# Optimization experiments

Hardware: AMD Instinct MI355X
Metric: run time of the kernel (lower is better)

## Reference

```python
import jax, jax.numpy as jnp
import numpy as np

B, C, H, W = 4, 512, 28, 28
HEADS, K, DIL = 16, 7, 1
DH = C // HEADS
EPS = 1e-5


def _nbr_idx(n):
    # NATTEN-style clamped windows: near borders the window shifts to stay in-bounds.
    span = DIL * (K - 1) + 1
    start = np.clip(np.arange(n) - (K // 2) * DIL, 0, n - span)
    idx = start[:, None] + np.arange(K) * DIL              # [n, K] absolute neighbor indices
    rel = (idx - np.arange(n)[:, None]) // DIL + (K - 1)    # [n, K] rpb indices in [0, 2K-2]
    return jnp.asarray(idx), jnp.asarray(rel)


def _batchnorm(x, gamma, beta):
    # x: [B, C, H, W]; training-mode BN (batch statistics, biased variance)
    mean = x.mean(axis=(0, 2, 3), keepdims=True)
    var = x.var(axis=(0, 2, 3), keepdims=True)
    xn = (x - mean) * jax.lax.rsqrt(var + EPS)
    return xn * gamma[None, :, None, None] + beta[None, :, None, None]


def _neighborhood_attn(xh, qkv_w, qkv_b, proj_w, proj_b, rpb):
    # xh: [B, H, W, C]
    qkv = jnp.einsum('bijc,oc->bijo', xh, qkv_w) + qkv_b          # [B,H,W,3C]
    qkv = qkv.reshape(B, H, W, 3, HEADS, DH)
    q = qkv[..., 0, :, :].transpose(0, 3, 1, 2, 4)                 # [B,heads,H,W,dh]
    k = qkv[..., 1, :, :].transpose(0, 3, 1, 2, 4)
    v = qkv[..., 2, :, :].transpose(0, 3, 1, 2, 4)

    idx_r, rel_r = _nbr_idx(H)
    idx_c, rel_c = _nbr_idx(W)

    def gather(t):  # [B,heads,H,W,dh] -> [B,heads,H,W,K*K,dh]
        t = t[:, :, idx_r]                 # [B,heads,H,K,W,dh]
        t = t[:, :, :, :, idx_c]           # [B,heads,H,K,W,K,dh]
        t = t.transpose(0, 1, 2, 4, 3, 5, 6)
        return t.reshape(B, HEADS, H, W, K * K, DH)

    kg = gather(k)
    vg = gather(v)

    scale = DH ** -0.5
    logits = jnp.einsum('bhijd,bhijnd->bhijn', q * scale, kg)      # [B,heads,H,W,K*K]

    # relative position bias: rpb[h, rel_r[i,a], rel_c[j,b]]
    bias = rpb[:, rel_r]                   # [heads,H,K,2K-1]
    bias = bias[:, :, :, rel_c]            # [heads,H,K,W,K]
    bias = bias.transpose(0, 1, 3, 2, 4).reshape(HEADS, H, W, K * K)
    logits = logits + bias[None]

    attn = jax.nn.softmax(logits, axis=-1)
    out = jnp.einsum('bhijn,bhijnd->bhijd', attn, vg)              # [B,heads,H,W,dh]
    out = out.transpose(0, 2, 3, 1, 4).reshape(B, H, W, C)
    return jnp.einsum('bijc,oc->bijo', out, proj_w) + proj_b


def setup_inputs() -> dict:
    key = jax.random.key(0)
    ks = jax.random.split(key, 8)
    p = lambda k_, shp: (jax.random.normal(k_, shp, jnp.float32) * 0.02)
    return {
        'x': jax.random.normal(ks[0], (B, C, H, W), jnp.float32),
        'qkv_w': p(ks[1], (3 * C, C)), 'qkv_b': jnp.zeros((3 * C,), jnp.float32),
        'proj_w': p(ks[2], (C, C)), 'proj_b': jnp.zeros((C,), jnp.float32),
        'rpb': p(ks[3], (HEADS, 2 * K - 1, 2 * K - 1)),
        'w1': p(ks[4], (2 * C, C)), 'b1': jnp.zeros((2 * C,), jnp.float32),
        'w2': p(ks[5], (C, 2 * C)), 'b2': jnp.zeros((C,), jnp.float32),
        'g1': jnp.ones((C,), jnp.float32), 'be1': jnp.zeros((C,), jnp.float32),
        'g2': jnp.ones((C,), jnp.float32), 'be2': jnp.zeros((C,), jnp.float32),
    }


def reference(x, qkv_w, qkv_b, proj_w, proj_b, rpb, w1, b1, w2, b2, g1, be1, g2, be2):
    xh = x.transpose(0, 2, 3, 1)                                   # NCHW -> NHWC
    h = _neighborhood_attn(xh, qkv_w, qkv_b, proj_w, proj_b, rpb)
    h = h.transpose(0, 3, 1, 2)                                    # back to NCHW
    x1 = _batchnorm(x + h, g1, be1)
    # FFN: 1x1 conv (C -> 2C), exact GELU, 1x1 conv (2C -> C)
    t = jnp.einsum('bchw,oc->bohw', x1, w1) + b1[None, :, None, None]
    t = jax.nn.gelu(t, approximate=False)
    h2 = jnp.einsum('bchw,oc->bohw', t, w2) + b2[None, :, None, None]
    return _batchnorm(x1 + h2, g2, be2)
```

## Files before the change

kernel.cpp:

```cpp
#include <hip/hip_runtime.h>
#include <hip/hip_bf16.h>
#include <math.h>

#define BATCH 4
#define CCH   512
#define HWPIX 784
#define NPIX  3136
#define MPAD  3200
#define EPS   1e-5f

using f32x4  = __attribute__((ext_vector_type(4))) float;
using bf16x8 = __attribute__((ext_vector_type(8))) __bf16;

__device__ __forceinline__ short f2b(float f) {
    unsigned u = __float_as_uint(f);
    unsigned r = (u + 0x7FFFu + ((u >> 16) & 1u)) >> 16;
    return (short)r;
}
__device__ __forceinline__ unsigned pk2(float a, float b) {
    return (unsigned)(unsigned short)f2b(a) | ((unsigned)(unsigned short)f2b(b) << 16);
}
__device__ __forceinline__ float bl(unsigned u)  { return __uint_as_float(u << 16); }
__device__ __forceinline__ float bh(unsigned u)  { return __uint_as_float(u & 0xffff0000u); }
__device__ __forceinline__ float b16f(short s) {
    return __uint_as_float((unsigned)(unsigned short)s << 16);
}

__device__ __forceinline__ void gload_lds16(const void* g, void* l) {
    __builtin_amdgcn_global_load_lds((const __attribute__((address_space(1))) void*)g,
                                     (__attribute__((address_space(3))) void*)l, 16, 0, 0);
}

__global__ __launch_bounds__(256) void k_prep(const float* __restrict__ qkv_w,
                                              const float* __restrict__ proj_w,
                                              const float* __restrict__ w2,
                                              const float* __restrict__ x,
                                              short* __restrict__ Wb,
                                              short* __restrict__ xhb) {
    __shared__ float tile[32][33];
    const int bid = blockIdx.x;
    if (bid < 1536) {
        int i = (bid * 256 + threadIdx.x) * 4;
        const float* src; int base;
        if (i < 786432)       { src = qkv_w;  base = 0; }
        else if (i < 1048576) { src = proj_w; base = 786432; }
        else                  { src = w2;     base = 1048576; }
        float4 v = *(const float4*)&src[i - base];
        *(uint2*)&Wb[i] = make_uint2(pk2(v.x, v.y), pk2(v.z, v.w));
        return;
    }
    const int t = bid - 1536;
    const int b = t / 400, r = t % 400;
    const int c0 = (r / 25) * 32, p0 = (r % 25) * 32;
    const int tx = threadIdx.x & 31, ty = threadIdx.x >> 5;
    for (int i = ty; i < 32; i += 8) {
        int c = c0 + i, p = p0 + tx;
        tile[i][tx] = (p < HWPIX) ? x[((size_t)b * CCH + c) * HWPIX + p] : 0.f;
    }
    __syncthreads();
    for (int i = ty; i < 32; i += 8) {
        int p = p0 + i, c = c0 + tx;
        if (p < HWPIX) xhb[((size_t)b * HWPIX + p) * CCH + c] = f2b(tile[tx][i]);
    }
}

template<int BM, int BN, int N, int K, int EPI, int OUTB, int STATS>
__global__ __launch_bounds__(512) void k_gemm_mfma(
        const short* __restrict__ A, const short* __restrict__ Bw,
        const float* __restrict__ bias, const short* __restrict__ resb,
        const float* __restrict__ ss,
        short* __restrict__ Cb, float* __restrict__ part) {
    constexpr int BK = 64;
    constexpr int KH = K / 2;
    constexpr int MR = BM / 32, NR = BN / 32;
    constexpr int AISS = BM / 32, BISS = BN / 32;
    constexpr int SCR = (BM / 2) * BN;
    __shared__ __align__(16) short As[2][BM * BK];
    __shared__ __align__(16) short Bs[2][BN * BK];
    const int tid   = threadIdx.x;
    const int half  = tid >> 8;
    const int tid_h = tid & 255;
    const int wid2  = (tid >> 6) & 3;
    const int lane  = tid & 63;
    const int wr    = wid2 >> 1, wc = wid2 & 1;
    const int m0    = blockIdx.x * BM, n0 = blockIdx.y * BN;
    const int srow  = tid_h >> 3;
    const int skcz  = (tid_h & 7) ^ (srow & 7);
    const int frow  = lane & 15;
    const int fk2   = (lane >> 4) * 16;

    f32x4 acc[MR][NR];
    const f32x4 vzero = {0.f, 0.f, 0.f, 0.f};
#pragma unroll
    for (int m = 0; m < MR; ++m)
#pragma unroll
        for (int n = 0; n < NR; ++n) acc[m][n] = vzero;

    const short* Ab = A  + (size_t)(m0 + srow) * K + skcz * 8 + half * KH;
    const short* Bb = Bw + (size_t)(n0 + srow) * K + skcz * 8 + half * KH;
    const char* Abase = (const char*)&As[half][0];
    const char* Bbase = (const char*)&Bs[half][0];

    for (int k0 = 0; k0 < KH; k0 += BK) {
#pragma unroll
        for (int it = 0; it < AISS; ++it)
            gload_lds16(Ab + (size_t)it * 32 * K + k0, &As[half][(it * 256 + wid2 * 64) * 8]);
#pragma unroll
        for (int it = 0; it < BISS; ++it)
            gload_lds16(Bb + (size_t)it * 32 * K + k0, &Bs[half][(it * 256 + wid2 * 64) * 8]);
        __syncthreads();
#pragma unroll
        for (int kk = 0; kk < 2; ++kk) {
            bf16x8 af[MR], bfr[NR];
#pragma unroll
            for (int m = 0; m < MR; ++m) {
                const int Ra = wr * (BM / 2) + m * 16 + frow;
                af[m] = *(const bf16x8*)(Abase + Ra * 128 + ((kk * 64 + fk2) ^ ((Ra & 7) << 4)));
            }
#pragma unroll
            for (int n = 0; n < NR; ++n) {
                const int Rb = wc * (BN / 2) + n * 16 + frow;
                bfr[n] = *(const bf16x8*)(Bbase + Rb * 128 + ((kk * 64 + fk2) ^ ((Rb & 7) << 4)));
            }
#pragma unroll
            for (int m = 0; m < MR; ++m)
#pragma unroll
                for (int n = 0; n < NR; ++n)
                    acc[m][n] = __builtin_amdgcn_mfma_f32_16x16x32_bf16(af[m], bfr[n], acc[m][n], 0, 0, 0);
        }
        __syncthreads();
    }

    const int crow0l = wr * (BM / 2) + (lane >> 4) * 4;
    const int ccol0l = wc * (BN / 2) + (lane & 15);
    float* scr = wr ? (float*)Bs : (float*)As;
    const int rbase = crow0l - wr * (BM / 2);
    if (half == 1) {
#pragma unroll
        for (int m = 0; m < MR; ++m)
#pragma unroll
            for (int n = 0; n < NR; ++n)
#pragma unroll
                for (int j = 0; j < 4; ++j)
                    scr[(rbase + m * 16 + j) * BN + ccol0l + n * 16] = acc[m][n][j];
    }
    __syncthreads();

    float ls[NR], ls2[NR];
#pragma unroll
    for (int n = 0; n < NR; ++n) { ls[n] = 0.f; ls2[n] = 0.f; }

    if (half == 0) {
#pragma unroll
        for (int m = 0; m < MR; ++m)
#pragma unroll
            for (int n = 0; n < NR; ++n)
#pragma unroll
                for (int j = 0; j < 4; ++j)
                    acc[m][n][j] += scr[(rbase + m * 16 + j) * BN + ccol0l + n * 16];
#pragma unroll
        for (int m = 0; m < MR; ++m) {
            const int row0 = m0 + crow0l + m * 16;
#pragma unroll
            for (int n = 0; n < NR; ++n) {
                const int col = n0 + ccol0l + n * 16;
                const float bv = bias[col];
#pragma unroll
                for (int j = 0; j < 4; ++j) {
                    const int row = row0 + j;
                    float v = acc[m][n][j] + bv;
                    if (EPI == 1) v = 0.5f * v * (1.0f + erff(v * 0.70710678118654752f));
                    if (EPI == 2) v += b16f(resb[(size_t)row * 512 + col]);
                    if (EPI == 3) v += fmaf(b16f(resb[(size_t)row * 512 + col]),
                                            ss[col], ss[CCH + col]);
                    if (OUTB) Cb[(size_t)row * N + col] = f2b(v);
                    if (STATS && row < NPIX) { ls[n] += v; ls2[n] = fmaf(v, v, ls2[n]); }
                }
            }
        }
    }
    if (STATS) {
        float* red  = (float*)Bs + SCR;
        float* red2 = red + 8 * BN;
        if (half == 0) {
            const int rrow = wr * 4 + (lane >> 4);
#pragma unroll
            for (int n = 0; n < NR; ++n) {
                int cslot = ccol0l + n * 16;
                red [rrow * BN + cslot] = ls[n];
                red2[rrow * BN + cslot] = ls2[n];
            }
        }
        __syncthreads();
        if (tid < BN) {
            float s = 0.f, s2 = 0.f;
#pragma unroll
            for (int r = 0; r < 8; ++r) { s += red[r * BN + tid]; s2 += red2[r * BN + tid]; }
            part[blockIdx.x * N + n0 + tid]          = s;
            part[50 * N + blockIdx.x * N + n0 + tid] = s2;
        }
    }
}

__global__ __launch_bounds__(256) void k_attn(const short* __restrict__ qkvb,
                                              const float* __restrict__ rpb,
                                              short* __restrict__ outb) {
    const int xcd = blockIdx.x & 7, bidx = blockIdx.x >> 3;
    const int eff = xcd * 98 + bidx;
    const int wid = threadIdx.x >> 6, lane = threadIdx.x & 63;
    const int pix = eff * 4 + wid;
    const int h = lane >> 2, d = lane & 3;
    const unsigned upix = (unsigned)pix;
    const int j = upix % 28u;
    const unsigned t2 = upix / 28u;
    const int i = t2 % 28u;
    const int b = t2 / 28u;
    const int si = min(max(i - 3, 0), 21), sj = min(max(j - 3, 0), 21);
    const int oi = si - i + 6, oj = sj - j + 6;
    const int pbase = b * HWPIX + si * 28 + sj;
    const int choff = h * 32 + d * 8;

    float q[8];
    {
        uint4 qu = *(const uint4*)(qkvb + (size_t)pix * 1536 + choff);
        const float sc = 0.17677669529663687f;
        q[0] = bl(qu.x) * sc; q[1] = bh(qu.x) * sc;
        q[2] = bl(qu.y) * sc; q[3] = bh(qu.y) * sc;
        q[4] = bl(qu.z) * sc; q[5] = bh(qu.z) * sc;
        q[6] = bl(qu.w) * sc; q[7] = bh(qu.w) * sc;
    }
    const short* kbase = qkvb + (size_t)pbase * 1536 + 512 + choff;
    const float* rb = rpb + h * 169 + oi * 13 + oj;

    float parr[13];
#pragma unroll
    for (int t = 0; t < 13; ++t) parr[t] = -1e30f;

#pragma unroll
    for (int kr = 0; kr < 7; ++kr) {
        const short* krow = kbase + kr * (28 * 1536);
        const float* brow = rb + kr * 13;
#pragma unroll
        for (int kc = 0; kc < 7; ++kc) {
            const int n = kr * 7 + kc;
            uint4 ku = *(const uint4*)(krow + kc * 1536);
            float dot = q[0] * bl(ku.x);
            dot = fmaf(q[1], bh(ku.x), dot);
            dot = fmaf(q[2], bl(ku.y), dot);
            dot = fmaf(q[3], bh(ku.y), dot);
            dot = fmaf(q[4], bl(ku.z), dot);
            dot = fmaf(q[5], bh(ku.z), dot);
            dot = fmaf(q[6], bl(ku.w), dot);
            dot = fmaf(q[7], bh(ku.w), dot);
            dot += __shfl_xor(dot, 1);
            dot += __shfl_xor(dot, 2);
            float lg = dot + brow[kc];
            if ((n & 3) == d) parr[n >> 2] = lg;
        }
    }
    float mx = parr[0];
#pragma unroll
    for (int t = 1; t < 13; ++t) mx = fmaxf(mx, parr[t]);
    mx = fmaxf(mx, __shfl_xor(mx, 1));
    mx = fmaxf(mx, __shfl_xor(mx, 2));
    float s = 0.f;
#pragma unroll
    for (int t = 0; t < 13; ++t) { float e = __expf(parr[t] - mx); parr[t] = e; s += e; }
    s += __shfl_xor(s, 1);
    s += __shfl_xor(s, 2);

    const short* vbase = qkvb + (size_t)pbase * 1536 + 1024 + choff;
    const int gbase = lane & 60;
    float o[8] = {0.f, 0.f, 0.f, 0.f, 0.f, 0.f, 0.f, 0.f};
#pragma unroll
    for (int kr = 0; kr < 7; ++kr) {
        const short* vrow = vbase + kr * (28 * 1536);
#pragma unroll
        for (int kc = 0; kc < 7; ++kc) {
            const int n = kr * 7 + kc;
            uint4 vu = *(const uint4*)(vrow + kc * 1536);
            float pn = __shfl(parr[n >> 2], gbase | (n & 3));
            o[0] = fmaf(pn, bl(vu.x), o[0]);
            o[1] = fmaf(pn, bh(vu.x), o[1]);
            o[2] = fmaf(pn, bl(vu.y), o[2]);
            o[3] = fmaf(pn, bh(vu.y), o[3]);
            o[4] = fmaf(pn, bl(vu.z), o[4]);
            o[5] = fmaf(pn, bh(vu.z), o[5]);
            o[6] = fmaf(pn, bl(vu.w), o[6]);
            o[7] = fmaf(pn, bh(vu.w), o[7]);
        }
    }
    const float rs = 1.f / s;
    uint4 ov;
    ov.x = pk2(o[0] * rs, o[1] * rs);
    ov.y = pk2(o[2] * rs, o[3] * rs);
    ov.z = pk2(o[4] * rs, o[5] * rs);
    ov.w = pk2(o[6] * rs, o[7] * rs);
    *(uint4*)&outb[(size_t)pix * 512 + choff] = ov;
}

__global__ __launch_bounds__(256) void k_fold_w1(const float* __restrict__ part,
                                                 const float* __restrict__ g,
                                                 const float* __restrict__ be,
                                                 const float* __restrict__ w1,
                                                 const float* __restrict__ b1,
                                                 short* __restrict__ w1s,
                                                 float* __restrict__ b1c,
                                                 float* __restrict__ ssout) {
    __shared__ float ssc[CCH], ssh[CCH];
    const int tid = threadIdx.x;
    for (int cc = tid; cc < CCH; cc += 256) {
        float s = 0.f, s2 = 0.f;
        for (int p = 0; p < 50; ++p) {
            s  += part[p * CCH + cc];
            s2 += part[50 * CCH + p * CCH + cc];
        }
        float mean = s * (1.0f / NPIX);
        float var  = s2 * (1.0f / NPIX) - mean * mean;
        float rstd = rsqrtf(var + EPS);
        float sc = rstd * g[cc], sh = be[cc] - mean * sc;
        ssc[cc] = sc; ssh[cc] = sh;
        if (blockIdx.x == 0) { ssout[cc] = sc; ssout[CCH + cc] = sh; }
    }
    __syncthreads();
    const int n = blockIdx.x * 4 + (tid >> 6);
    const int lane = tid & 63;
    const int c = lane * 8;
    const float* wr = w1 + (size_t)n * CCH + c;
    float4 wa = *(const float4*)wr, wb = *(const float4*)(wr + 4);
    float4 sa = *(const float4*)&ssc[c], sb = *(const float4*)&ssc[c + 4];
    float4 ha = *(const float4*)&ssh[c], hb = *(const float4*)&ssh[c + 4];
    uint4 o;
    o.x = pk2(wa.x * sa.x, wa.y * sa.y);
    o.y = pk2(wa.z * sa.z, wa.w * sa.w);
    o.z = pk2(wb.x * sb.x, wb.y * sb.y);
    o.w = pk2(wb.z * sb.z, wb.w * sb.w);
    *(uint4*)&w1s[(size_t)n * CCH + c] = o;
    float p = wa.x * ha.x + wa.y * ha.y + wa.z * ha.z + wa.w * ha.w
            + wb.x * hb.x + wb.y * hb.y + wb.z * hb.z + wb.w * hb.w;
#pragma unroll
    for (int off = 32; off >= 1; off >>= 1) p += __shfl_xor(p, off);
    if (lane == 0) b1c[n] = b1[n] + p;
}

__global__ __launch_bounds__(256) void k_bn2_out(const short* __restrict__ y,
                                                 const float* __restrict__ part,
                                                 const float* __restrict__ g,
                                                 const float* __restrict__ be,
                                                 float* __restrict__ out) {
    __shared__ float tile[32][33];
    __shared__ float red[2][8][32];
    __shared__ float ssc[32], ssh[32];
    const int b  = blockIdx.z;
    const int p0 = blockIdx.y * 32;
    const int c0 = blockIdx.x * 32;
    const int tx = threadIdx.x & 31, ty = threadIdx.x >> 5;
    {
        const int c = c0 + tx;
        float s = 0.f, s2 = 0.f;
        for (int p = ty; p < 50; p += 8) {
            s  += part[p * CCH + c];
            s2 += part[50 * CCH + p * CCH + c];
        }
        red[0][ty][tx] = s; red[1][ty][tx] = s2;
    }
    __syncthreads();
    if (ty == 0) {
        float s = 0.f, s2 = 0.f;
#pragma unroll
        for (int r = 0; r < 8; ++r) { s += red[0][r][tx]; s2 += red[1][r][tx]; }
        float mean = s * (1.0f / NPIX);
        float var  = s2 * (1.0f / NPIX) - mean * mean;
        float rstd = rsqrtf(var + EPS);
        float sc = rstd * g[c0 + tx];
        ssc[tx] = sc; ssh[tx] = be[c0 + tx] - mean * sc;
    }
    __syncthreads();
    for (int i = ty; i < 32; i += 8) {
        int p = p0 + i, c = c0 + tx;
        float v = 0.f;
        if (p < HWPIX) v = fmaf(b16f(y[((size_t)b * HWPIX + p) * CCH + c]), ssc[tx], ssh[tx]);
        tile[i][tx] = v;
    }
    __syncthreads();
    for (int i = ty; i < 32; i += 8) {
        int c = c0 + i, p = p0 + tx;
        if (p < HWPIX) out[((size_t)b * CCH + c) * HWPIX + p] = tile[tx][i];
    }
}

extern "C" void kernel_launch(void* const* d_in, const int* in_sizes, int n_in,
                              void* d_out, int out_size, void* d_ws, size_t ws_size,
                              hipStream_t stream) {
    const float* x      = (const float*)d_in[0];
    const float* qkv_w  = (const float*)d_in[1];
    const float* qkv_b  = (const float*)d_in[2];
    const float* proj_w = (const float*)d_in[3];
    const float* proj_b = (const float*)d_in[4];
    const float* rpb    = (const float*)d_in[5];
    const float* w1     = (const float*)d_in[6];
    const float* b1     = (const float*)d_in[7];
    const float* w2     = (const float*)d_in[8];
    const float* b2     = (const float*)d_in[9];
    const float* g1     = (const float*)d_in[10];
    const float* be1    = (const float*)d_in[11];
    const float* g2     = (const float*)d_in[12];
    const float* be2    = (const float*)d_in[13];
    float* out = (float*)d_out;

    float* ws    = (float*)d_ws;
    short* XHb   = (short*)(ws);
    short* QKVb  = (short*)(ws + 819200);
    short* Tb    = QKVb;
    short* ATTb  = (short*)(ws + 3276800);
    short* Y1b   = (short*)(ws + 4096000);
    short* Y2b   = (short*)(ws + 4915200);
    short* Wb    = (short*)(ws + 5734400);
    short* Wqkv  = Wb;
    short* Wproj = Wb + 786432;
    short* W2b   = Wb + 1048576;
    short* W1s   = Wb + 1572864;
    float* PART  = ws + 6782976;
    float* SS1   = ws + 6834176;
    float* B1c   = ws + 6835200;

    k_prep<<<3136, 256, 0, stream>>>(qkv_w, proj_w, w2, x, Wb, XHb);
    k_gemm_mfma<64, 128, 1536, 512, 0, 1, 0>
        <<<dim3(50, 12), 512, 0, stream>>>(XHb, Wqkv, qkv_b, nullptr, nullptr,
                                           QKVb, nullptr);
    k_attn<<<784, 256, 0, stream>>>(QKVb, rpb, ATTb);
    k_gemm_mfma<64, 64, 512, 512, 2, 1, 1>
        <<<dim3(50, 8), 512, 0, stream>>>(ATTb, Wproj, proj_b, XHb, nullptr,
                                          Y1b, PART);
    k_fold_w1<<<256, 256, 0, stream>>>(PART, g1, be1, w1, b1, W1s, B1c, SS1);
    k_gemm_mfma<64, 128, 1024, 512, 1, 1, 0>
        <<<dim3(50, 8), 512, 0, stream>>>(Y1b, W1s, B1c, nullptr, nullptr,
                                          Tb, nullptr);
    k_gemm_mfma<64, 64, 512, 1024, 3, 1, 1>
        <<<dim3(50, 8), 512, 0, stream>>>(Tb, W2b, b2, Y1b, SS1,
                                          Y2b, PART);
    k_bn2_out<<<dim3(16, 25, BATCH), 256, 0, stream>>>(Y2b, PART, g2, be2, out);
}
```

Before: 95.86 us.

## Use a 128x128-tile GEMM kernel for the QKV and FFN1 projections

Adds a new GEMM kernel using 128x128 tiles, 4 waves each computing a 64x64 sub-tile with 16x16x32 bf16 MFMAs, and XOR-swizzled LDS loaded via direct global-to-LDS copies. It replaces the older 64x128 split-K-style kernel for the QKV and first FFN GEMMs. The aim is more data reuse per tile and fewer blocks. The trade-off is that the new kernel has a single LDS buffer with no double buffering, so loads are not overlapped with compute. It also launches fewer blocks (300 and 200), which may underfill the GPU's compute units.

```diff
diff --git a/kernel.cpp b/kernel.cpp
--- a/kernel.cpp
+++ b/kernel.cpp
@@ -61,6 +61,82 @@
     for (int i = ty; i < 32; i += 8) {
         int p = p0 + i, c = c0 + tx;
         if (p < HWPIX) xhb[((size_t)b * HWPIX + p) * CCH + c] = f2b(tile[tx][i]);
+    }
+}
+
+template<int N, int K, int EPI>
+__global__ __launch_bounds__(256) void k_gemm128(
+        const short* __restrict__ A, const short* __restrict__ Bw,
+        const float* __restrict__ bias, short* __restrict__ Cb) {
+    constexpr int BM = 128, BN = 128, BK = 64;
+    __shared__ __align__(16) short As[BM * BK];
+    __shared__ __align__(16) short Bs[BN * BK];
+    const int tid  = threadIdx.x;
+    const int wid  = tid >> 6, lane = tid & 63;
+    const int wr   = wid >> 1, wc = wid & 1;
+    const int m0   = blockIdx.x * BM, n0 = blockIdx.y * BN;
+    const int srow = tid >> 3;
+    const int skcz = (tid & 7) ^ (srow & 7);
+    const int frow = lane & 15;
+    const int fk2  = (lane >> 4) * 16;
+
+    f32x4 acc[4][4];
+    const f32x4 vzero = {0.f, 0.f, 0.f, 0.f};
+#pragma unroll
+    for (int m = 0; m < 4; ++m)
+#pragma unroll
+        for (int n = 0; n < 4; ++n) acc[m][n] = vzero;
+
+    const short* Ab = A  + (size_t)(m0 + srow) * K + skcz * 8;
+    const short* Bb = Bw + (size_t)(n0 + srow) * K + skcz * 8;
+    const char* Abase = (const char*)As;
+    const char* Bbase = (const char*)Bs;
+
+    for (int k0 = 0; k0 < K; k0 += BK) {
+#pragma unroll
+        for (int it = 0; it < 4; ++it)
+            gload_lds16(Ab + (size_t)it * 32 * K + k0, &As[(it * 32 + srow) * BK + (tid & 7) * 8]);
+#pragma unroll
+        for (int it = 0; it < 4; ++it)
+            gload_lds16(Bb + (size_t)it * 32 * K + k0, &Bs[(it * 32 + srow) * BK + (tid & 7) * 8]);
+        __syncthreads();
+#pragma unroll
+        for (int kk = 0; kk < 2; ++kk) {
+            bf16x8 af[4], bfr[4];
+#pragma unroll
+            for (int m = 0; m < 4; ++m) {
+                const int Ra = wr * 64 + m * 16 + frow;
+                af[m] = *(const bf16x8*)(Abase + Ra * 128 + ((kk * 64 + fk2) ^ ((Ra & 7) << 4)));
+            }
+#pragma unroll
+            for (int n = 0; n < 4; ++n) {
+                const int Rb = wc * 64 + n * 16 + frow;
+                bfr[n] = *(const bf16x8*)(Bbase + Rb * 128 + ((kk * 64 + fk2) ^ ((Rb & 7) << 4)));
+            }
+#pragma unroll
+            for (int m = 0; m < 4; ++m)
+#pragma unroll
+                for (int n = 0; n < 4; ++n)
+                    acc[m][n] = __builtin_amdgcn_mfma_f32_16x16x32_bf16(af[m], bfr[n], acc[m][n], 0, 0, 0);
+        }
+        __syncthreads();
+    }
+    const int crow0 = m0 + wr * 64 + (lane >> 4) * 4;
+    const int ccol0 = n0 + wc * 64 + (lane & 15);
+#pragma unroll
+    for (int m = 0; m < 4; ++m) {
+#pragma unroll
+        for (int n = 0; n < 4; ++n) {
+            const int col = ccol0 + n * 16;
+            const float bv = bias[col];
+#pragma unroll
+            for (int j = 0; j < 4; ++j) {
+                const int row = crow0 + m * 16 + j;
+                float v = acc[m][n][j] + bv;
+                if (EPI == 1) v = 0.5f * v * (1.0f + erff(v * 0.70710678118654752f));
+                Cb[(size_t)row * N + col] = f2b(v);
+            }
+        }
     }
 }
 
@@ -425,17 +501,15 @@
     float* B1c   = ws + 6835200;
 
     k_prep<<<3136, 256, 0, stream>>>(qkv_w, proj_w, w2, x, Wb, XHb);
-    k_gemm_mfma<64, 128, 1536, 512, 0, 1, 0>
-        <<<dim3(50, 12), 512, 0, stream>>>(XHb, Wqkv, qkv_b, nullptr, nullptr,
-                                           QKVb, nullptr);
+    k_gemm128<1536, 512, 0>
+        <<<dim3(25, 12), 256, 0, stream>>>(XHb, Wqkv, qkv_b, QKVb);
     k_attn<<<784, 256, 0, stream>>>(QKVb, rpb, ATTb);
     k_gemm_mfma<64, 64, 512, 512, 2, 1, 1>
         <<<dim3(50, 8), 512, 0, stream>>>(ATTb, Wproj, proj_b, XHb, nullptr,
                                           Y1b, PART);
     k_fold_w1<<<256, 256, 0, stream>>>(PART, g1, be1, w1, b1, W1s, B1c, SS1);
-    k_gemm_mfma<64, 128, 1024, 512, 1, 1, 0>
-        <<<dim3(50, 8), 512, 0, stream>>>(Y1b, W1s, B1c, nullptr, nullptr,
-                                          Tb, nullptr);
+    k_gemm128<1024, 512, 1>
+        <<<dim3(25, 8), 256, 0, stream>>>(Y1b, W1s, B1c, Tb);
     k_gemm_mfma<64, 64, 512, 1024, 3, 1, 1>
         <<<dim3(50, 8), 512, 0, stream>>>(Tb, W2b, b2, Y1b, SS1,
                                           Y2b, PART);
```

Measured after the change: 103.1 us. 1.08x slower.

## Stage K/V neighborhood rows in double-buffered LDS shared across block pixels

Applied to the files above, without the earlier changes.

The neighborhood attention kernel now cooperatively loads each K and V window row for the block's four adjacent pixels into shared memory. It uses async global-to-LDS copies with double buffering, and each wave then reads its 7 neighbors from LDS. Before, every wave fetched its 49 neighbors straight from global memory. The goal is to cut redundant global/L2 traffic from overlapping windows and to overlap the next row's load with the current row's compute. In exchange it adds a block-wide barrier per window row and drops full unrolling of the row loop.

```diff
diff --git a/kernel.cpp b/kernel.cpp
--- a/kernel.cpp
+++ b/kernel.cpp
@@ -205,45 +205,66 @@
 __global__ __launch_bounds__(256) void k_attn(const short* __restrict__ qkvb,
                                               const float* __restrict__ rpb,
                                               short* __restrict__ outb) {
+    __shared__ __align__(16) short Kst[2][5120];
     const int xcd = blockIdx.x & 7, bidx = blockIdx.x >> 3;
     const int eff = xcd * 98 + bidx;
     const int wid = threadIdx.x >> 6, lane = threadIdx.x & 63;
-    const int pix = eff * 4 + wid;
+    const int pixb = eff * 4;
+    const int pix  = pixb + wid;
+    const int j0 = pixb % 28;
+    const int t2 = pixb / 28;
+    const int i  = t2 % 28;
+    const int b  = t2 / 28;
+    const int j  = j0 + wid;
+    const int si  = min(max(i - 3, 0), 21);
+    const int sj0 = min(max(j0 - 3, 0), 21);
+    const int sj3 = min(max(j0, 0), 21);
+    const int Wt  = sj3 - sj0 + 7;
+    const int offw = min(max(j - 3, 0), 21) - sj0;
+    const int oi = si - i + 6;
+    const int oj = sj0 + offw - j + 6;
+    const int rowb0 = b * HWPIX + si * 28 + sj0;
     const int h = lane >> 2, d = lane & 3;
-    const unsigned upix = (unsigned)pix;
-    const int j = upix % 28u;
-    const unsigned t2 = upix / 28u;
-    const int i = t2 % 28u;
-    const int b = t2 / 28u;
-    const int si = min(max(i - 3, 0), 21), sj = min(max(j - 3, 0), 21);
-    const int oi = si - i + 6, oj = sj - j + 6;
-    const int pbase = b * HWPIX + si * 28 + sj;
-    const int choff = h * 32 + d * 8;
 
     float q[8];
     {
-        uint4 qu = *(const uint4*)(qkvb + (size_t)pix * 1536 + choff);
+        uint4 qu = *(const uint4*)(qkvb + (size_t)pix * 1536 + lane * 8);
         const float sc = 0.17677669529663687f;
         q[0] = bl(qu.x) * sc; q[1] = bh(qu.x) * sc;
         q[2] = bl(qu.y) * sc; q[3] = bh(qu.y) * sc;
         q[4] = bl(qu.z) * sc; q[5] = bh(qu.z) * sc;
         q[6] = bl(qu.w) * sc; q[7] = bh(qu.w) * sc;
     }
-    const short* kbase = qkvb + (size_t)pbase * 1536 + 512 + choff;
     const float* rb = rpb + h * 169 + oi * 13 + oj;
+    const int wlim = Wt * 64;
+
+    auto STG = [&](int kr, int bufi, int kvoff) {
+        const short* src = qkvb + (size_t)(rowb0 + kr * 28) * 1536 + kvoff;
+#pragma unroll
+        for (int r = 0; r < 3; ++r) {
+            const int c0 = r * 256 + wid * 64;
+            if (c0 < wlim) {
+                const int c = c0 + lane;
+                gload_lds16(src + (size_t)(c >> 6) * 1536 + (c & 63) * 8,
+                            &Kst[bufi][c * 8]);
+            }
+        }
+    };
 
     float parr[13];
 #pragma unroll
     for (int t = 0; t < 13; ++t) parr[t] = -1e30f;
 
-#pragma unroll
+    STG(0, 0, 512);
+    __syncthreads();
     for (int kr = 0; kr < 7; ++kr) {
-        const short* krow = kbase + kr * (28 * 1536);
+        if (kr < 6) STG(kr + 1, (kr + 1) & 1, 512);
+        const short* kb = &Kst[kr & 1][0];
         const float* brow = rb + kr * 13;
 #pragma unroll
         for (int kc = 0; kc < 7; ++kc) {
             const int n = kr * 7 + kc;
-            uint4 ku = *(const uint4*)(krow + kc * 1536);
+            uint4 ku = *(const uint4*)(kb + (offw + kc) * 512 + lane * 8);
             float dot = q[0] * bl(ku.x);
             dot = fmaf(q[1], bh(ku.x), dot);
             dot = fmaf(q[2], bl(ku.y), dot);
@@ -257,7 +278,9 @@
             float lg = dot + brow[kc];
             if ((n & 3) == d) parr[n >> 2] = lg;
         }
-    }
+        __syncthreads();
+    }
+
     float mx = parr[0];
 #pragma unroll
     for (int t = 1; t < 13; ++t) mx = fmaxf(mx, parr[t]);
@@ -269,16 +292,17 @@
     s += __shfl_xor(s, 1);
     s += __shfl_xor(s, 2);
 
-    const short* vbase = qkvb + (size_t)pbase * 1536 + 1024 + choff;
     const int gbase = lane & 60;
     float o[8] = {0.f, 0.f, 0.f, 0.f, 0.f, 0.f, 0.f, 0.f};
-#pragma unroll
+    STG(0, 0, 1024);
+    __syncthreads();
     for (int kr = 0; kr < 7; ++kr) {
-        const short* vrow = vbase + kr * (28 * 1536);
+        if (kr < 6) STG(kr + 1, (kr + 1) & 1, 1024);
+        const short* vb = &Kst[kr & 1][0];
 #pragma unroll
         for (int kc = 0; kc < 7; ++kc) {
             const int n = kr * 7 + kc;
-            uint4 vu = *(const uint4*)(vrow + kc * 1536);
+            uint4 vu = *(const uint4*)(vb + (offw + kc) * 512 + lane * 8);
             float pn = __shfl(parr[n >> 2], gbase | (n & 3));
             o[0] = fmaf(pn, bl(vu.x), o[0]);
             o[1] = fmaf(pn, bh(vu.x), o[1]);
@@ -289,6 +313,7 @@
             o[6] = fmaf(pn, bl(vu.w), o[6]);
             o[7] = fmaf(pn, bh(vu.w), o[7]);
         }
+        __syncthreads();
     }
     const float rs = 1.f / s;
     uint4 ov;
@@ -296,7 +321,7 @@
     ov.y = pk2(o[2] * rs, o[3] * rs);
     ov.z = pk2(o[4] * rs, o[5] * rs);
     ov.w = pk2(o[6] * rs, o[7] * rs);
-    *(uint4*)&outb[(size_t)pix * 512 + choff] = ov;
+    *(uint4*)&outb[(size_t)pix * 512 + lane * 8] = ov;
 }
 
 __global__ __launch_bounds__(256) void k_fold_w1(const float* __restrict__ part,
```

New measurement: 103.2 us. 1.08x slower.
